# Performance work log

Hardware: AMD Instinct MI355X
Metric: run time of the kernel (lower is better)

Reference implementation:

```python
import jax, jax.numpy as jnp
import numpy as np

B, D, H, W = 64, 64, 32, 32
K = 1024


def setup_inputs() -> dict:
    key = jax.random.key(0)
    k1, k2 = jax.random.split(key)
    latents = jax.random.normal(k1, (B, D, H, W), dtype=jnp.float32)
    # nn.Embedding(K, D) initialized uniform(-1/K, 1/K)
    embedding = jax.random.uniform(k2, (K, D), dtype=jnp.float32,
                                   minval=-1.0 / K, maxval=1.0 / K)
    return {"latents": latents, "embedding": embedding}


def reference(latents, embedding):
    # [B, D, H, W] -> [B, H, W, D]
    x = jnp.transpose(latents, (0, 2, 3, 1))
    x_shape = x.shape
    flat = x.reshape(-1, x_shape[-1])  # [N, D], N = B*H*W
    # squared euclidean distances to each code: [N, K]
    dist = (jnp.sum(flat ** 2, axis=1, keepdims=True)
            + jnp.sum(embedding ** 2, axis=1)
            - 2.0 * flat @ embedding.T)
    encoding_inds = jnp.argmin(dist, axis=1)  # [N]
    # gather codes (equivalent to one_hot @ embedding)
    quantized = embedding[encoding_inds].reshape(x_shape)  # [B, H, W, D]
    commitment_loss = jnp.mean((jax.lax.stop_gradient(quantized) - x) ** 2)
    embedding_loss = jnp.mean((quantized - jax.lax.stop_gradient(x)) ** 2)
    # straight-through estimator
    quantized_st = x + jax.lax.stop_gradient(quantized - x)
    q_out = jnp.transpose(quantized_st, (0, 3, 1, 2))  # [B, D, H, W]
    return q_out, commitment_loss, embedding_loss, encoding_inds
```

## Files before the change

### kernel.cpp

```cpp
#include <hip/hip_runtime.h>

#define QSIZE 4194304
#define WS_E2_OFF   0
#define WS_ET_OFF   4096
#define WS_PART_OFF 266240

__global__ void k0_e2(const float* __restrict__ emb, float* __restrict__ e2) {
    #pragma clang fp contract(off)
    int k = blockIdx.x * blockDim.x + threadIdx.x;
    if (k >= 1024) return;
    const float* e = emb + k * 64;
    float r[8];
    #pragma unroll
    for (int j = 0; j < 8; ++j) r[j] = e[j] * e[j];
    #pragma unroll
    for (int i = 8; i < 64; i += 8) {
        #pragma unroll
        for (int j = 0; j < 8; ++j) r[j] = r[j] + e[i + j] * e[i + j];
    }
    e2[k] = ((r[0] + r[1]) + (r[2] + r[3])) + ((r[4] + r[5]) + (r[6] + r[7]));
}

__global__ void k0_tr(const float* __restrict__ emb, float* __restrict__ embT) {
    int g = blockIdx.x * 256 + threadIdx.x;
    int d = g >> 10, k = g & 1023;
    embT[g] = emb[k * 64 + d];
}

__launch_bounds__(256, 4)
__global__ void k1_argmin(const float* __restrict__ lat, const float* __restrict__ embT,
                          const float* __restrict__ e2t, const float* __restrict__ emb,
                          float* __restrict__ out, float* __restrict__ part) {
    #pragma clang fp contract(off)
    __shared__ float2 xs2[32][64];
    __shared__ float sm1[4][64];
    __shared__ int   sbi[4][64];
    __shared__ int   sbiF[64];
    __shared__ float red[4];

    const int tid  = threadIdx.x;
    const int lane = tid & 63;
    const int w    = tid >> 6;
    const int row0 = blockIdx.x * 64;
    const int row  = row0 + lane;
    const int b    = row >> 10;
    const int hw   = row & 1023;

    {
        const int hwb = row0 & 1023;
        const float* latb = lat + (size_t)b * 65536 + hwb;
        #pragma unroll
        for (int i = 0; i < 16; ++i) {
            const int idx = i * 256 + tid;
            const int d = idx >> 6, r = idx & 63;
            const float v = latb[d * 1024 + r];
            ((float*)&xs2[d >> 1][r])[d & 1] = v;
        }
    }
    __syncthreads();

    float x2;
    {
        float r[8];
        #pragma unroll
        for (int j = 0; j < 8; ++j) {
            const float v = ((const float*)&xs2[j >> 1][lane])[j & 1];
            r[j] = v * v;
        }
        #pragma unroll
        for (int i = 8; i < 64; i += 8) {
            #pragma unroll
            for (int j = 0; j < 8; ++j) {
                const float v = ((const float*)&xs2[(i + j) >> 1][lane])[(i + j) & 1];
                r[j] = r[j] + v * v;
            }
        }
        x2 = ((r[0] + r[1]) + (r[2] + r[3])) + ((r[4] + r[5]) + (r[6] + r[7]));
    }

    const int kbase = __builtin_amdgcn_readfirstlane(w) << 8;
    float m1 = 3.4e38f;
    int   bi = kbase;
    #pragma unroll 1
    for (int g = 0; g < 16; ++g) {
        const int k0 = kbase + (g << 4);
        const float* __restrict__ ed  = embT + k0;
        const float* __restrict__ e2g = e2t + k0;
        float c[16];
        #pragma unroll
        for (int j = 0; j < 16; ++j) c[j] = 0.f;
        #pragma unroll 2
        for (int dd = 0; dd < 32; ++dd) {
            const float2 xv = xs2[dd][lane];
            const float* e0 = ed + (dd << 11);
            #pragma unroll
            for (int j = 0; j < 16; ++j) c[j] = __builtin_fmaf(xv.x, e0[j], c[j]);
            const float* e1 = e0 + 1024;
            #pragma unroll
            for (int j = 0; j < 16; ++j) c[j] = __builtin_fmaf(xv.y, e1[j], c[j]);
        }
        #pragma unroll
        for (int j = 0; j < 16; ++j) {
            const float t  = x2 + e2g[j];
            const float dv = t - 2.0f * c[j];
            if (dv < m1) { m1 = dv; bi = k0 + j; }
        }
    }
    sm1[w][lane] = m1;
    sbi[w][lane] = bi;
    __syncthreads();

    if (w == 0) {
        float M1 = sm1[0][lane];
        int   BI = sbi[0][lane];
        #pragma unroll
        for (int ww = 1; ww < 4; ++ww) {
            const float a = sm1[ww][lane];
            if (a < M1) { M1 = a; BI = sbi[ww][lane]; }
        }
        sbiF[lane] = BI;
        out[QSIZE + 2 + row] = (float)BI;
    }
    __syncthreads();

    {
        const float* xg = lat + (size_t)b * 65536 + hw;
        const int BI = sbiF[lane];
        const float* er = emb + BI * 64 + w * 16;
        float sq = 0.f;
        #pragma unroll
        for (int j4 = 0; j4 < 4; ++j4) {
            const float4 q4 = *(const float4*)(er + j4 * 4);
            #pragma unroll
            for (int j2 = 0; j2 < 4; ++j2) {
                const int d = w * 16 + j4 * 4 + j2;
                const float xv  = xg[d * 1024];
                const float qv  = (&q4.x)[j2];
                const float qmx = qv - xv;
                out[(size_t)b * 65536 + d * 1024 + hw] = xv + qmx;
                sq = __builtin_fmaf(qmx, qmx, sq);
            }
        }
        #pragma unroll
        for (int off = 32; off > 0; off >>= 1) sq += __shfl_down(sq, off, 64);
        if (lane == 0) red[w] = sq;
    }
    __syncthreads();
    if (tid == 0) part[blockIdx.x] = (red[0] + red[1]) + (red[2] + red[3]);
}

__global__ void k3_final(const float* __restrict__ part, float* __restrict__ out) {
    __shared__ double red[256];
    double s = 0.0;
    for (int i = threadIdx.x; i < 1024; i += 256) s += (double)part[i];
    red[threadIdx.x] = s;
    __syncthreads();
    for (int st = 128; st > 0; st >>= 1) {
        if (threadIdx.x < st) red[threadIdx.x] += red[threadIdx.x + st];
        __syncthreads();
    }
    if (threadIdx.x == 0) {
        float L = (float)(red[0] / (double)QSIZE);
        out[QSIZE]     = L;
        out[QSIZE + 1] = L;
    }
}

extern "C" void kernel_launch(void* const* d_in, const int* in_sizes, int n_in,
                              void* d_out, int out_size, void* d_ws, size_t ws_size,
                              hipStream_t stream) {
    const float* lat = (const float*)d_in[0];
    const float* emb = (const float*)d_in[1];
    float* out  = (float*)d_out;
    char*  ws   = (char*)d_ws;
    float* e2t  = (float*)(ws + WS_E2_OFF);
    float* embT = (float*)(ws + WS_ET_OFF);
    float* part = (float*)(ws + WS_PART_OFF);

    hipLaunchKernelGGL(k0_e2,     dim3(4),    dim3(256), 0, stream, emb, e2t);
    hipLaunchKernelGGL(k0_tr,     dim3(256),  dim3(256), 0, stream, emb, embT);
    hipLaunchKernelGGL(k1_argmin, dim3(1024), dim3(256), 0, stream, lat, embT, e2t, emb, out, part);
    hipLaunchKernelGGL(k3_final,  dim3(1),    dim3(256), 0, stream, part, out);
}
```

Measured before the change: 186.6 us.

## Merge prep kernels, use 8 waves per block, packed FMA, atomic loss reduction

Folds the embedding transpose and norm kernels into one launch and removes the final reduction kernel. Loss partials are now accumulated with atomicAdd into zero-initialised outputs. The argmin kernel moves to 512 threads per block, so each wave scans 128 codes instead of 256. The distance dot products use 2-wide vector FMA, which can map to packed FP32 FMA. These changes aim to cut launch overhead and raise parallelism within each block, at the cost of nondeterministic float atomics in the loss and more register pressure from the full dd unroll.

```diff
diff --git a/kernel.cpp b/kernel.cpp
--- a/kernel.cpp
+++ b/kernel.cpp
@@ -3,40 +3,45 @@
 #define QSIZE 4194304
 #define WS_E2_OFF   0
 #define WS_ET_OFF   4096
-#define WS_PART_OFF 266240
 
-__global__ void k0_e2(const float* __restrict__ emb, float* __restrict__ e2) {
+typedef float f2 __attribute__((ext_vector_type(2)));
+
+__global__ void k0_prep(const float* __restrict__ emb, float* __restrict__ embT,
+                        float* __restrict__ e2, float* __restrict__ out) {
     #pragma clang fp contract(off)
-    int k = blockIdx.x * blockDim.x + threadIdx.x;
-    if (k >= 1024) return;
-    const float* e = emb + k * 64;
-    float r[8];
-    #pragma unroll
-    for (int j = 0; j < 8; ++j) r[j] = e[j] * e[j];
-    #pragma unroll
-    for (int i = 8; i < 64; i += 8) {
-        #pragma unroll
-        for (int j = 0; j < 8; ++j) r[j] = r[j] + e[i + j] * e[i + j];
+    if (blockIdx.x < 256) {
+        int g = blockIdx.x * 256 + threadIdx.x;
+        int d = g >> 10, k = g & 1023;
+        embT[g] = emb[k * 64 + d];
+    } else {
+        #pragma unroll 1
+        for (int j = 0; j < 4; ++j) {
+            int k = j * 256 + threadIdx.x;
+            const float* e = emb + k * 64;
+            float r[8];
+            #pragma unroll
+            for (int q = 0; q < 8; ++q) r[q] = e[q] * e[q];
+            #pragma unroll
+            for (int i = 8; i < 64; i += 8) {
+                #pragma unroll
+                for (int q = 0; q < 8; ++q) r[q] = r[q] + e[i + q] * e[i + q];
+            }
+            e2[k] = ((r[0] + r[1]) + (r[2] + r[3])) + ((r[4] + r[5]) + (r[6] + r[7]));
+        }
+        if (threadIdx.x < 2) out[QSIZE + threadIdx.x] = 0.f;
     }
-    e2[k] = ((r[0] + r[1]) + (r[2] + r[3])) + ((r[4] + r[5]) + (r[6] + r[7]));
 }
 
-__global__ void k0_tr(const float* __restrict__ emb, float* __restrict__ embT) {
-    int g = blockIdx.x * 256 + threadIdx.x;
-    int d = g >> 10, k = g & 1023;
-    embT[g] = emb[k * 64 + d];
-}
-
-__launch_bounds__(256, 4)
+__launch_bounds__(512, 8)
 __global__ void k1_argmin(const float* __restrict__ lat, const float* __restrict__ embT,
                           const float* __restrict__ e2t, const float* __restrict__ emb,
-                          float* __restrict__ out, float* __restrict__ part) {
+                          float* __restrict__ out) {
     #pragma clang fp contract(off)
-    __shared__ float2 xs2[32][64];
-    __shared__ float sm1[4][64];
-    __shared__ int   sbi[4][64];
+    __shared__ f2    xs2[32][64];
+    __shared__ float sm1[8][64];
+    __shared__ int   sbi[8][64];
     __shared__ int   sbiF[64];
-    __shared__ float red[4];
+    __shared__ float red[8];
 
     const int tid  = threadIdx.x;
     const int lane = tid & 63;
@@ -47,14 +52,12 @@
     const int hw   = row & 1023;
 
     {
-        const int hwb = row0 & 1023;
-        const float* latb = lat + (size_t)b * 65536 + hwb;
+        const float* latb = lat + (size_t)b * 65536 + (row0 & 1023);
         #pragma unroll
-        for (int i = 0; i < 16; ++i) {
-            const int idx = i * 256 + tid;
+        for (int i = 0; i < 8; ++i) {
+            const int idx = i * 512 + tid;
             const int d = idx >> 6, r = idx & 63;
-            const float v = latb[d * 1024 + r];
-            ((float*)&xs2[d >> 1][r])[d & 1] = v;
+            ((float*)&xs2[d >> 1][r])[d & 1] = latb[d * 1024 + r];
         }
     }
     __syncthreads();
@@ -63,47 +66,50 @@
     {
         float r[8];
         #pragma unroll
-        for (int j = 0; j < 8; ++j) {
-            const float v = ((const float*)&xs2[j >> 1][lane])[j & 1];
-            r[j] = v * v;
-        }
+        for (int q = 0; q < 8; ++q) r[q] = 0.f;
         #pragma unroll
-        for (int i = 8; i < 64; i += 8) {
-            #pragma unroll
-            for (int j = 0; j < 8; ++j) {
-                const float v = ((const float*)&xs2[(i + j) >> 1][lane])[(i + j) & 1];
-                r[j] = r[j] + v * v;
-            }
+        for (int i = 0; i < 64; i += 8) {
+            const f2 p0 = xs2[(i >> 1) + 0][lane];
+            const f2 p1 = xs2[(i >> 1) + 1][lane];
+            const f2 p2 = xs2[(i >> 1) + 2][lane];
+            const f2 p3 = xs2[(i >> 1) + 3][lane];
+            r[0] = r[0] + p0.x * p0.x;  r[1] = r[1] + p0.y * p0.y;
+            r[2] = r[2] + p1.x * p1.x;  r[3] = r[3] + p1.y * p1.y;
+            r[4] = r[4] + p2.x * p2.x;  r[5] = r[5] + p2.y * p2.y;
+            r[6] = r[6] + p3.x * p3.x;  r[7] = r[7] + p3.y * p3.y;
         }
         x2 = ((r[0] + r[1]) + (r[2] + r[3])) + ((r[4] + r[5]) + (r[6] + r[7]));
     }
 
-    const int kbase = __builtin_amdgcn_readfirstlane(w) << 8;
+    const int kbase = __builtin_amdgcn_readfirstlane(w) << 7;
     float m1 = 3.4e38f;
     int   bi = kbase;
     #pragma unroll 1
-    for (int g = 0; g < 16; ++g) {
-        const int k0 = kbase + (g << 4);
-        const float* __restrict__ ed  = embT + k0;
-        const float* __restrict__ e2g = e2t + k0;
-        float c[16];
+    for (int g = 0; g < 8; ++g) {
+        const int k0c = kbase + (g << 4);
+        f2 c2[8];
         #pragma unroll
-        for (int j = 0; j < 16; ++j) c[j] = 0.f;
-        #pragma unroll 2
+        for (int j = 0; j < 8; ++j) c2[j] = (f2){0.f, 0.f};
+        #pragma unroll
         for (int dd = 0; dd < 32; ++dd) {
-            const float2 xv = xs2[dd][lane];
-            const float* e0 = ed + (dd << 11);
+            const f2 xv = xs2[dd][lane];
+            const f2* __restrict__ e0 = (const f2*)(embT + (dd << 11) + k0c);
+            const f2 xl = {xv.x, xv.x};
             #pragma unroll
-            for (int j = 0; j < 16; ++j) c[j] = __builtin_fmaf(xv.x, e0[j], c[j]);
-            const float* e1 = e0 + 1024;
+            for (int j = 0; j < 8; ++j) c2[j] = __builtin_elementwise_fma(e0[j], xl, c2[j]);
+            const f2* __restrict__ e1 = e0 + 512;
+            const f2 xh = {xv.y, xv.y};
             #pragma unroll
-            for (int j = 0; j < 16; ++j) c[j] = __builtin_fmaf(xv.y, e1[j], c[j]);
+            for (int j = 0; j < 8; ++j) c2[j] = __builtin_elementwise_fma(e1[j], xh, c2[j]);
         }
         #pragma unroll
-        for (int j = 0; j < 16; ++j) {
-            const float t  = x2 + e2g[j];
-            const float dv = t - 2.0f * c[j];
-            if (dv < m1) { m1 = dv; bi = k0 + j; }
+        for (int j = 0; j < 8; ++j) {
+            const float ta = x2 + e2t[k0c + 2 * j];
+            const float da = ta - 2.0f * c2[j].x;
+            if (da < m1) { m1 = da; bi = k0c + 2 * j; }
+            const float tb = x2 + e2t[k0c + 2 * j + 1];
+            const float db = tb - 2.0f * c2[j].y;
+            if (db < m1) { m1 = db; bi = k0c + 2 * j + 1; }
         }
     }
     sm1[w][lane] = m1;
@@ -114,7 +120,7 @@
         float M1 = sm1[0][lane];
         int   BI = sbi[0][lane];
         #pragma unroll
-        for (int ww = 1; ww < 4; ++ww) {
+        for (int ww = 1; ww < 8; ++ww) {
             const float a = sm1[ww][lane];
             if (a < M1) { M1 = a; BI = sbi[ww][lane]; }
         }
@@ -126,14 +132,14 @@
     {
         const float* xg = lat + (size_t)b * 65536 + hw;
         const int BI = sbiF[lane];
-        const float* er = emb + BI * 64 + w * 16;
+        const float* er = emb + BI * 64 + w * 8;
         float sq = 0.f;
         #pragma unroll
-        for (int j4 = 0; j4 < 4; ++j4) {
+        for (int j4 = 0; j4 < 2; ++j4) {
             const float4 q4 = *(const float4*)(er + j4 * 4);
             #pragma unroll
             for (int j2 = 0; j2 < 4; ++j2) {
-                const int d = w * 16 + j4 * 4 + j2;
+                const int d = w * 8 + j4 * 4 + j2;
                 const float xv  = xg[d * 1024];
                 const float qv  = (&q4.x)[j2];
                 const float qmx = qv - xv;
@@ -146,23 +152,11 @@
         if (lane == 0) red[w] = sq;
     }
     __syncthreads();
-    if (tid == 0) part[blockIdx.x] = (red[0] + red[1]) + (red[2] + red[3]);
-}
-
-__global__ void k3_final(const float* __restrict__ part, float* __restrict__ out) {
-    __shared__ double red[256];
-    double s = 0.0;
-    for (int i = threadIdx.x; i < 1024; i += 256) s += (double)part[i];
-    red[threadIdx.x] = s;
-    __syncthreads();
-    for (int st = 128; st > 0; st >>= 1) {
-        if (threadIdx.x < st) red[threadIdx.x] += red[threadIdx.x + st];
-        __syncthreads();
-    }
-    if (threadIdx.x == 0) {
-        float L = (float)(red[0] / (double)QSIZE);
-        out[QSIZE]     = L;
-        out[QSIZE + 1] = L;
+    if (tid == 0) {
+        const float p = (((red[0] + red[1]) + (red[2] + red[3]))
+                       + ((red[4] + red[5]) + (red[6] + red[7]))) * (1.0f / 4194304.0f);
+        atomicAdd(&out[QSIZE],     p);
+        atomicAdd(&out[QSIZE + 1], p);
     }
 }
 
@@ -175,10 +169,7 @@
     char*  ws   = (char*)d_ws;
     float* e2t  = (float*)(ws + WS_E2_OFF);
     float* embT = (float*)(ws + WS_ET_OFF);
-    float* part = (float*)(ws + WS_PART_OFF);
 
-    hipLaunchKernelGGL(k0_e2,     dim3(4),    dim3(256), 0, stream, emb, e2t);
-    hipLaunchKernelGGL(k0_tr,     dim3(256),  dim3(256), 0, stream, emb, embT);
-    hipLaunchKernelGGL(k1_argmin, dim3(1024), dim3(256), 0, stream, lat, embT, e2t, emb, out, part);
-    hipLaunchKernelGGL(k3_final,  dim3(1),    dim3(256), 0, stream, part, out);
+    hipLaunchKernelGGL(k0_prep,   dim3(257),  dim3(256), 0, stream, emb, embT, e2t, out);
+    hipLaunchKernelGGL(k1_argmin, dim3(1024), dim3(512), 0, stream, lat, embT, e2t, emb, out);
 }
```

New measurement: 334.8 us. 1.79x slower.
